# Kernel optimization log

Hardware: AMD Instinct MI355X
Metric: run time of the kernel (lower is better)

Reference implementation:

```python
import jax, jax.numpy as jnp
import numpy as np

S, T, F, J, E, H = 1024, 64, 128, 64, 256, 4
DH = E // H


def layer_norm(x, g, b, eps=1e-10):
    m = jnp.mean(x, axis=-1, keepdims=True)
    v = jnp.mean((x - m) ** 2, axis=-1, keepdims=True)  # population var (correction=0)
    return (x - m) / jnp.sqrt(v + eps) * g + b


def mha(x, Wq, Wk, Wv):
    # x: [B, L, E]; Wq/Wk/Wv: [H, E, DH]. Non-standard: scale AFTER softmax@V.
    q = jnp.einsum('ble,hed->hbld', x, Wq)
    k = jnp.einsum('ble,hed->hbld', x, Wk)
    v = jnp.einsum('ble,hed->hbld', x, Wv)
    w = jax.nn.softmax(jnp.einsum('hbld,hbmd->hblm', q, k), axis=-1)
    o = jnp.einsum('hblm,hbmd->hbld', w, v) / jnp.sqrt(jnp.asarray(Wq.shape[-1], x.dtype))
    h, b, l, d = o.shape
    return jnp.transpose(o, (1, 2, 0, 3)).reshape(b, l, h * d)


def ffn(x, W1, b1, W2, b2):
    return jnp.maximum(x @ W1 + b1, 0.0) @ W2 + b2  # Dropout is identity in eval


def pos_encoding(t, e):
    pos = jnp.arange(t, dtype=jnp.float32)[:, None]
    two_i = jnp.floor(jnp.arange(e, dtype=jnp.float32) / 2.0) * 2.0
    div = jnp.power(jnp.float32(100004.0), two_i / e)
    pe = pos / div  # [t, e]
    pe = pe.at[:, 0::2].set(jnp.sin(pe[:, 0::2]))
    pe = pe.at[:, 1::2].set(jnp.cos(pe[:, 1::2]))
    return pe


def setup_inputs() -> dict:
    key = jax.random.key(0)
    ks = jax.random.split(key, 32)
    s = 0.02
    d = {}
    d['x'] = jax.random.normal(ks[0], (S, T, F + J), dtype=jnp.float32)
    d['gate_W'] = s * jax.random.normal(ks[1], (J, F))
    d['gate_b'] = s * jax.random.normal(ks[2], (F,))
    d['embed_W'] = s * jax.random.normal(ks[3], (F, E))
    d['ln0_g'] = 1.0 + s * jax.random.normal(ks[4], (E,))
    d['ln0_b'] = s * jax.random.normal(ks[5], (E,))
    d['intra_Wq'] = s * jax.random.normal(ks[6], (H, E, DH))
    d['intra_Wk'] = s * jax.random.normal(ks[7], (H, E, DH))
    d['intra_Wv'] = s * jax.random.normal(ks[8], (H, E, DH))
    d['intra_ln_g'] = 1.0 + s * jax.random.normal(ks[9], (E,))
    d['intra_ln_b'] = s * jax.random.normal(ks[10], (E,))
    d['intra_W1'] = s * jax.random.normal(ks[11], (E, 4 * E))
    d['intra_b1'] = s * jax.random.normal(ks[12], (4 * E,))
    d['intra_W2'] = s * jax.random.normal(ks[13], (4 * E, E))
    d['intra_b2'] = s * jax.random.normal(ks[14], (E,))
    d['inter_Wq'] = s * jax.random.normal(ks[15], (H, E, DH))
    d['inter_Wk'] = s * jax.random.normal(ks[16], (H, E, DH))
    d['inter_Wv'] = s * jax.random.normal(ks[17], (H, E, DH))
    d['inter_ln1_g'] = 1.0 + s * jax.random.normal(ks[18], (E,))
    d['inter_ln1_b'] = s * jax.random.normal(ks[19], (E,))
    d['inter_ln2_g'] = 1.0 + s * jax.random.normal(ks[20], (E,))
    d['inter_ln2_b'] = s * jax.random.normal(ks[21], (E,))
    d['inter_W1'] = s * jax.random.normal(ks[22], (E, 4 * E))
    d['inter_b1'] = s * jax.random.normal(ks[23], (4 * E,))
    d['inter_W2'] = s * jax.random.normal(ks[24], (4 * E, E))
    d['inter_b2'] = s * jax.random.normal(ks[25], (E,))
    d['temp_W'] = s * jax.random.normal(ks[26], (E, E))
    d['pred_W'] = s * jax.random.normal(ks[27], (E, 1))
    d['pred_b'] = s * jax.random.normal(ks[28], (1,))
    return d


def reference(x, gate_W, gate_b, embed_W, ln0_g, ln0_b,
              intra_Wq, intra_Wk, intra_Wv, intra_ln_g, intra_ln_b,
              intra_W1, intra_b1, intra_W2, intra_b2,
              inter_Wq, inter_Wk, inter_Wv, inter_ln1_g, inter_ln1_b,
              inter_ln2_g, inter_ln2_b, inter_W1, inter_b1, inter_W2, inter_b2,
              temp_W, pred_W, pred_b):
    # Gating
    x_f = x[..., :F]                       # [S, T, F]
    x_g = x[..., -1, F:]                   # [S, J]
    gate = jax.nn.softmax(x_g @ gate_W + gate_b, axis=-1)[:, None, :]
    x_f = gate * x_f
    # Embed + positional encoding + LN
    emb = x_f @ embed_W                    # [S, T, E]
    res = emb + pos_encoding(T, E)
    ln = layer_norm(res, ln0_g, ln0_b)
    # Intra-stock attention (attend over time axis per stock)
    a = mha(ln, intra_Wq, intra_Wk, intra_Wv)
    r = a + ln
    intra_out = r + ffn(layer_norm(r, intra_ln_g, intra_ln_b), intra_W1, intra_b1, intra_W2, intra_b2)
    # Inter-stock attention (attend over stock axis per timestep)
    xT = jnp.transpose(intra_out, (1, 0, 2))            # [T, S, E]
    xTn = layer_norm(xT, inter_ln1_g, inter_ln1_b)
    a2 = mha(xTn, inter_Wq, inter_Wk, inter_Wv)          # [T, S, E]
    out = jnp.transpose(a2, (1, 0, 2))                   # [S, T, E]
    r2 = out + intra_out
    inter_out = r2 + ffn(layer_norm(r2, inter_ln2_g, inter_ln2_b), inter_W1, inter_b1, inter_W2, inter_b2)
    # Temporal aggregation
    x1 = inter_out @ temp_W                              # [S, T, E]
    cur = x1[..., -1, :][..., :, None]                   # [S, E, 1]
    lam = jax.nn.softmax(jnp.squeeze(x1 @ cur, -1), axis=-1)[:, None, :]  # [S, 1, T]
    agg = jnp.squeeze(lam @ inter_out, -2)               # [S, E]
    # Prediction
    return agg @ pred_W + pred_b                         # [S, 1]
```

## Files before the change

kernel.cpp:

```cpp
#include <hip/hip_runtime.h>


typedef _Float16 h16;
typedef __attribute__((ext_vector_type(8))) _Float16 f16x8;
typedef __attribute__((ext_vector_type(4))) _Float16 f16x4;
typedef __attribute__((ext_vector_type(4))) float f32x4;

__device__ inline float wave_sum(float v){
  #pragma unroll
  for (int o=32;o;o>>=1) v += __shfl_xor(v,o);
  return v;
}
__device__ inline float wave_max(float v){
  #pragma unroll
  for (int o=32;o;o>>=1) v = fmaxf(v,__shfl_xor(v,o));
  return v;
}

__global__ __launch_bounds__(256) void k_pe(float* __restrict__ pe){
  int t = blockIdx.x, i = threadIdx.x;
  float two_i = (float)((i>>1)<<1);
  float dv = powf(100004.0f, two_i*(1.0f/256.0f));
  float v = (float)t / dv;
  pe[t*256+i] = (i&1) ? cosf(v) : sinf(v);
}

__global__ __launch_bounds__(64) void k_gate(const float* __restrict__ x,
    const float* __restrict__ gW, const float* __restrict__ gb,
    float* __restrict__ gate){
  int s = blockIdx.x, lane = threadIdx.x;
  __shared__ float xg[64];
  xg[lane] = x[((size_t)s*64+63)*192 + 128 + lane];
  __syncthreads();
  float a0 = gb[lane], a1 = gb[64+lane];
  #pragma unroll 4
  for (int j=0;j<64;j++){
    float xv = xg[j];
    a0 += xv*gW[j*128+lane];
    a1 += xv*gW[j*128+64+lane];
  }
  float mx = wave_max(fmaxf(a0,a1));
  float e0 = __expf(a0-mx), e1 = __expf(a1-mx);
  float sm = wave_sum(e0+e1);
  gate[s*128+lane]    = e0/sm;
  gate[s*128+64+lane] = e1/sm;
}

__global__ __launch_bounds__(256) void k_t16all(
    const float* __restrict__ q1, const float* __restrict__ k1, const float* __restrict__ v1,
    const float* __restrict__ q2, const float* __restrict__ k2, const float* __restrict__ v2,
    const float* __restrict__ embed_W, const float* __restrict__ temp_W,
    const float* __restrict__ iW1, const float* __restrict__ iW2,
    const float* __restrict__ eW1, const float* __restrict__ eW2,
    h16* __restrict__ base){
  __shared__ float tile[32][33];
  const int b = blockIdx.x, tid = threadIdx.x;
  const float* src; h16* dst; int K, N, tb; bool qkv = false;
  if (b < 384){
    int mat = b>>6; tb = b&63; qkv = true; K = 256; N = 256;
    src = (mat==0)?q1:(mat==1)?k1:(mat==2)?v1:(mat==3)?q2:(mat==4)?k2:v2;
    dst = base + mat*65536;
  } else if (b < 416){ tb = b-384;  K=128;  N=256;  src=embed_W; dst=base+393216; }
  else if (b < 480){ tb = b-416;  K=256;  N=256;  src=temp_W;  dst=base+425984; }
  else if (b < 736){ tb = b-480;  K=256;  N=1024; src=iW1;     dst=base+491520; }
  else if (b < 992){ tb = b-736;  K=1024; N=256;  src=iW2;     dst=base+753664; }
  else if (b < 1248){ tb = b-992; K=256;  N=1024; src=eW1;     dst=base+1015808; }
  else               { tb = b-1248; K=1024; N=256; src=eW2;    dst=base+1277952; }
  const int nt = N>>5;
  const int N0 = (tb & (nt-1))<<5;
  const int K0 = (tb/nt)<<5;
  {
    int r = tid>>3, c0 = (tid&7)<<2;
    int k = K0+r, n = N0+c0;
    const float* p = qkv ? (src + ((n>>6)<<14) + (k<<6) + (n&63))
                         : (src + (size_t)k*N + n);
    float4 v = *(const float4*)p;
    tile[r][c0]=v.x; tile[r][c0+1]=v.y; tile[r][c0+2]=v.z; tile[r][c0+3]=v.w;
  }
  __syncthreads();
  {
    int r = tid>>3, c0 = (tid&7)<<2;
    f16x4 o;
    o[0]=(h16)tile[c0][r]; o[1]=(h16)tile[c0+1][r];
    o[2]=(h16)tile[c0+2][r]; o[3]=(h16)tile[c0+3][r];
    *(f16x4*)(dst + (size_t)(N0+r)*K + K0 + c0) = o;
  }
}

__global__ __launch_bounds__(256) void k_embed(
    const float* __restrict__ x, const h16* __restrict__ Et,
    const float* __restrict__ pe, const float* __restrict__ gate,
    const float* __restrict__ g0, const float* __restrict__ b0,
    float* __restrict__ A){
  __shared__ char pool[65536];
  h16*  As  = (h16*)pool;
  float* res = (float*)pool;
  const int tid = threadIdx.x, lane = tid&63, w = tid>>6;
  const int lr = lane&15, g = lane>>4;
  const int m0 = blockIdx.x<<6;
  #pragma unroll
  for (int it=0; it<8; it++){
    int f4 = it*256 + tid;
    int row = f4>>5, c4 = (f4&31)<<2;
    float4 v = *(const float4*)(x + (size_t)(m0+row)*192 + c4);
    float4 gg = *(const float4*)(gate + (((m0+row)>>6)<<7) + c4);
    v.x*=gg.x; v.y*=gg.y; v.z*=gg.z; v.w*=gg.w;
    int idx = ((row<<7) + c4) ^ ((row&7)<<3);
    f16x4 o; o[0]=(h16)v.x; o[1]=(h16)v.y; o[2]=(h16)v.z; o[3]=(h16)v.w;
    *(f16x4*)&As[idx] = o;
  }
  __syncthreads();
  f32x4 acc[4][4];
  #pragma unroll
  for (int a=0;a<4;a++)
    #pragma unroll
    for (int b=0;b<4;b++) acc[a][b] = (f32x4){0,0,0,0};
  #pragma unroll
  for (int kt=0; kt<4; kt++){
    f16x8 af[4], bf[4];
    #pragma unroll
    for (int rf=0; rf<4; rf++){
      int r = (rf<<4) + lr;
      int idx = ((r<<7) + (kt<<5) + (g<<3)) ^ ((r&7)<<3);
      af[rf] = *(const f16x8*)&As[idx];
    }
    #pragma unroll
    for (int cf=0; cf<4; cf++){
      int n = (w<<6) + (cf<<4) + lr;
      bf[cf] = *(const f16x8*)(Et + (size_t)n*128 + (kt<<5) + (g<<3));
    }
    #pragma unroll
    for (int rf=0; rf<4; rf++)
      #pragma unroll
      for (int cf=0; cf<4; cf++)
        acc[rf][cf] = __builtin_amdgcn_mfma_f32_16x16x32_f16(af[rf], bf[cf], acc[rf][cf], 0,0,0);
  }
  __syncthreads();
  #pragma unroll
  for (int cf=0; cf<4; cf++){
    int col = (w<<6) + (cf<<4) + lr;
    #pragma unroll
    for (int rf=0; rf<4; rf++)
      #pragma unroll
      for (int i=0;i<4;i++){
        int r = (rf<<4) + (g<<2) + i;
        res[(r<<8) + col] = acc[rf][cf][i] + pe[(r<<8) + col];
      }
  }
  __syncthreads();
  {
    float4 gg = *(const float4*)(g0 + (lane<<2));
    float4 bb = *(const float4*)(b0 + (lane<<2));
    for (int rr=0; rr<16; rr++){
      int r = (w<<4) + rr;
      float4 v = *(float4*)&res[(r<<8) + (lane<<2)];
      float sm = wave_sum(v.x+v.y+v.z+v.w);
      float sq = wave_sum(v.x*v.x+v.y*v.y+v.z*v.z+v.w*v.w);
      float mean = sm*(1.f/256.f);
      float rs = rsqrtf(sq*(1.f/256.f) - mean*mean + 1e-10f);
      float4 o;
      o.x=(v.x-mean)*rs*gg.x+bb.x; o.y=(v.y-mean)*rs*gg.y+bb.y;
      o.z=(v.z-mean)*rs*gg.z+bb.z; o.w=(v.w-mean)*rs*gg.w+bb.w;
      *(float4*)(A + (size_t)(m0+r)*256 + (lane<<2)) = o;
    }
  }
}

template<bool DOLN>
__global__ __launch_bounds__(512) void k_qkv(
    const float* __restrict__ X,
    const float* __restrict__ lng, const float* __restrict__ lnb,
    const h16* __restrict__ Bt0,
    h16* __restrict__ Qh, h16* __restrict__ Kh, h16* __restrict__ Vh){
  __shared__ h16 Xs[64*256];
  const int tid = threadIdx.x, lane = tid&63, w = tid>>6;
  const int lr = lane&15, g = lane>>4;
  const int m0 = blockIdx.x<<6;
  {
    float4 gg, bb;
    if (DOLN){ gg = *(const float4*)(lng + (lane<<2)); bb = *(const float4*)(lnb + (lane<<2)); }
    #pragma unroll
    for (int rr=0; rr<8; rr++){
      int r = (w<<3) + rr;
      float4 v = *(const float4*)(X + (size_t)(m0+r)*256 + (lane<<2));
      if (DOLN){
        float sm = wave_sum(v.x+v.y+v.z+v.w);
        float sq = wave_sum(v.x*v.x+v.y*v.y+v.z*v.z+v.w*v.w);
        float mean = sm*(1.f/256.f);
        float rs = rsqrtf(sq*(1.f/256.f) - mean*mean + 1e-10f);
        v.x=(v.x-mean)*rs*gg.x+bb.x; v.y=(v.y-mean)*rs*gg.y+bb.y;
        v.z=(v.z-mean)*rs*gg.z+bb.z; v.w=(v.w-mean)*rs*gg.w+bb.w;
      }
      f16x4 o; o[0]=(h16)v.x; o[1]=(h16)v.y; o[2]=(h16)v.z; o[3]=(h16)v.w;
      int idx = ((r<<8) + (lane<<2)) ^ ((r&7)<<3);
      *(f16x4*)&Xs[idx] = o;
    }
  }
  __syncthreads();
  f32x4 acc[4][3];
  #pragma unroll
  for (int a=0;a<4;a++)
    #pragma unroll
    for (int m=0;m<3;m++) acc[a][m] = (f32x4){0,0,0,0};
  #pragma unroll
  for (int kt=0; kt<8; kt++){
    f16x8 af[4], bf[3];
    #pragma unroll
    for (int rf=0; rf<4; rf++){
      int r = (rf<<4) + lr;
      int idx = ((r<<8) + (kt<<5) + (g<<3)) ^ ((r&7)<<3);
      af[rf] = *(const f16x8*)&Xs[idx];
    }
    #pragma unroll
    for (int m=0;m<3;m++){
      int n = (w<<4) + lr;
      bf[m] = *(const f16x8*)(Bt0 + (size_t)m*65536 + (size_t)n*256 + (kt<<5) + (g<<3));
    }
    #pragma unroll
    for (int rf=0; rf<4; rf++)
      #pragma unroll
      for (int m=0;m<3;m++)
        acc[rf][m] = __builtin_amdgcn_mfma_f32_16x16x32_f16(af[rf], bf[m], acc[rf][m], 0,0,0);
  }
  const int col = (w<<4) + lr;
  #pragma unroll
  for (int m=0;m<3;m++){
    h16* dst = (m==0)?Qh:(m==1)?Kh:Vh;
    #pragma unroll
    for (int rf=0; rf<4; rf++)
      #pragma unroll
      for (int i=0;i<4;i++){
        int r = m0 + (rf<<4) + (g<<2) + i;
        dst[(size_t)r*128 + col] = (h16)acc[rf][m][i];
      }
  }
}

template<int KDIM, int NB, int MODE>
__global__ __launch_bounds__(256) void k_gemm16(
    const float* __restrict__ A, int lda,
    const h16* __restrict__ Bt,
    void* __restrict__ Cv,
    const float* __restrict__ pe, const float* __restrict__ gate,
    size_t bstride, size_t cstride){
  __shared__ h16 As[64*KDIM];
  const int tid = threadIdx.x, lane = tid&63, w = tid>>6;
  const int lr = lane&15, g = lane>>4;
  const int m0 = blockIdx.x<<6;
  Bt += (size_t)blockIdx.y * bstride;
  constexpr int CF = NB/64;
  constexpr int KT = KDIM/32;
  #pragma unroll
  for (int it=0; it<16; it++){
    int f4 = it*256 + tid;
    int row = f4>>6, c4 = (f4&63)<<2;
    float4 v = *(const float4*)(A + (size_t)(m0+row)*lda + c4);
    int idx = ((row<<8) + c4) ^ ((row&7)<<3);
    f16x4 o; o[0]=(h16)v.x; o[1]=(h16)v.y; o[2]=(h16)v.z; o[3]=(h16)v.w;
    *(f16x4*)&As[idx] = o;
  }
  __syncthreads();
  f32x4 acc[4][CF];
  #pragma unroll
  for (int rf=0;rf<4;rf++)
    #pragma unroll
    for (int cf=0;cf<CF;cf++) acc[rf][cf] = (f32x4){0,0,0,0};
  #pragma unroll
  for (int kt=0; kt<KT; kt++){
    f16x8 af[4], bf[CF];
    #pragma unroll
    for (int rf=0; rf<4; rf++){
      int r = (rf<<4) + lr;
      int idx = (r*KDIM + (kt<<5) + (g<<3)) ^ ((r&7)<<3);
      af[rf] = *(const f16x8*)&As[idx];
    }
    #pragma unroll
    for (int cf=0; cf<CF; cf++){
      int n = w*(NB/4) + (cf<<4) + lr;
      bf[cf] = *(const f16x8*)(Bt + (size_t)n*KDIM + (kt<<5) + (g<<3));
    }
    #pragma unroll
    for (int rf=0; rf<4; rf++)
      #pragma unroll
      for (int cf=0; cf<CF; cf++)
        acc[rf][cf] = __builtin_amdgcn_mfma_f32_16x16x32_f16(af[rf], bf[cf], acc[rf][cf], 0,0,0);
  }
  #pragma unroll
  for (int cf=0; cf<CF; cf++){
    int col = w*(NB/4) + (cf<<4) + lr;
    #pragma unroll
    for (int rf=0; rf<4; rf++)
      #pragma unroll
      for (int i=0;i<4;i++){
        int m = m0 + (rf<<4) + (g<<2) + i;
        ((float*)Cv)[(size_t)m*256 + col] = acc[rf][cf][i];
      }
  }
}

template<int NT, int QG>
__global__ __launch_bounds__(256) void k_attn16(
    const h16* __restrict__ Qh, const h16* __restrict__ Kh, const h16* __restrict__ Vh,
    const float* __restrict__ Resid, float* __restrict__ Out, int hbase){
  __shared__ h16 Ks[64*64];
  __shared__ h16 VsT[64*64];
  __shared__ h16 Ps[4*QG*16*64];
  const int tid = threadIdx.x, lane = tid&63, w = tid>>6;
  const int lr = lane&15, g = lane>>4;
  int hh, t=0, qc=0, s=0;
  if (NT==1){ s = blockIdx.x; hh = blockIdx.y; }
  else      { hh = blockIdx.x; t = blockIdx.y; qc = blockIdx.z; }
  const int ccol = hh<<6;
  const int gcol = (hbase+hh)<<6;

  f16x8 qf[QG][2];
  #pragma unroll
  for (int grp=0; grp<QG; grp++){
    int ql = grp*64 + (w<<4) + lr;
    size_t m = (NT==1) ? ((size_t)s*64 + ql) : (((size_t)qc*(64*QG) + ql)*64 + t);
    const h16* qp = Qh + m*128 + ccol + (g<<3);
    qf[grp][0] = *(const f16x8*)qp;
    qf[grp][1] = *(const f16x8*)(qp + 32);
  }

  f32x4 oc[QG][4];
  float m_r[QG], l_r[QG];
  #pragma unroll
  for (int grp=0; grp<QG; grp++){
    #pragma unroll
    for (int cf=0;cf<4;cf++) oc[grp][cf] = (f32x4){0,0,0,0};
    m_r[grp] = -1e30f; l_r[grp] = 0.f;
  }

  for (int kb=0; kb<NT; kb++){
    __syncthreads();
    #pragma unroll
    for (int it=0; it<2; it++){
      int u = it*256 + tid;
      int row = u>>3, un = u&7;
      size_t m = (NT==1) ? ((size_t)s*64 + row) : (((size_t)kb*64 + row)*64 + t);
      f16x8 kv = *(const f16x8*)(Kh + m*128 + ccol + (un<<3));
      *(f16x8*)&Ks[(row<<6) + ((un ^ (row&7))<<3)] = kv;
      f16x8 vv = *(const f16x8*)(Vh + m*128 + ccol + (un<<3));
      #pragma unroll
      for (int j=0;j<8;j++){
        int d = (un<<3) + j;
        int key = (d + un) & 7;
        VsT[(d<<6) + ((((row>>3) ^ key))<<3) + (row&7)] = vv[j];
      }
    }
    __syncthreads();
    #pragma unroll
    for (int grp=0; grp<QG; grp++){
      f32x4 sa[4];
      #pragma unroll
      for (int mm=0;mm<4;mm++) sa[mm] = (f32x4){0,0,0,0};
      #pragma unroll
      for (int ks=0; ks<2; ks++){
        #pragma unroll
        for (int mm=0;mm<4;mm++){
          int krow = (mm<<4) + lr;
          f16x8 af = *(const f16x8*)&Ks[(krow<<6) + (((g + (ks<<2)) ^ (krow&7))<<3)];
          sa[mm] = __builtin_amdgcn_mfma_f32_16x16x32_f16(af, qf[grp][ks], sa[mm], 0,0,0);
        }
      }
      float pmax = -1e30f;
      #pragma unroll
      for (int mm=0;mm<4;mm++)
        #pragma unroll
        for (int i=0;i<4;i++) pmax = fmaxf(pmax, sa[mm][i]);
      pmax = fmaxf(pmax, __shfl_xor(pmax, 16));
      pmax = fmaxf(pmax, __shfl_xor(pmax, 32));
      float mn = fmaxf(m_r[grp], pmax);
      float sca = __expf(m_r[grp] - mn);
      m_r[grp] = mn;
      float ps = 0.f;
      f16x4 pv[4];
      #pragma unroll
      for (int mm=0;mm<4;mm++){
        #pragma unroll
        for (int i=0;i<4;i++){
          float p = __expf(sa[mm][i] - mn);
          ps += p;
          pv[mm][i] = (h16)p;
        }
      }
      ps += __shfl_xor(ps, 16);
      ps += __shfl_xor(ps, 32);
      l_r[grp] = l_r[grp]*sca + ps;
      const int pbase = ((w*QG + grp)<<10);
      #pragma unroll
      for (int mm=0;mm<4;mm++){
        int k0 = (mm<<4) + (g<<2);
        int unit = k0>>3, off = k0&7;
        *(f16x4*)&Ps[pbase + (lr<<6) + ((unit ^ (lr&7))<<3) + off] = pv[mm];
      }
      #pragma unroll
      for (int i=0;i<4;i++){
        float si = __shfl(sca, (g<<4) + (g<<2) + i);
        #pragma unroll
        for (int cf=0;cf<4;cf++) oc[grp][cf][i] *= si;
      }
      #pragma unroll
      for (int ks=0; ks<2; ks++){
        f16x8 pa = *(const f16x8*)&Ps[pbase + (lr<<6) + (((g + (ks<<2)) ^ (lr&7))<<3)];
        #pragma unroll
        for (int cf=0;cf<4;cf++){
          int d = (cf<<4) + lr;
          int key = (d + (d>>3)) & 7;
          f16x8 bf = *(const f16x8*)&VsT[(d<<6) + (((g + (ks<<2)) ^ key)<<3)];
          oc[grp][cf] = __builtin_amdgcn_mfma_f32_16x16x32_f16(pa, bf, oc[grp][cf], 0,0,0);
        }
      }
    }
  }
  #pragma unroll
  for (int grp=0; grp<QG; grp++){
    float linv = 1.0f/(l_r[grp]*8.0f);
    #pragma unroll
    for (int i=0;i<4;i++){
      float li = __shfl(linv, (g<<4) + (g<<2) + i);
      int ql = grp*64 + (w<<4) + (g<<2) + i;
      size_t m = (NT==1) ? ((size_t)s*64 + ql) : (((size_t)qc*(64*QG) + ql)*64 + t);
      #pragma unroll
      for (int cf=0;cf<4;cf++){
        int d = (cf<<4) + lr;
        size_t ga = m*256 + gcol + d;
        Out[ga] = oc[grp][cf][i]*li + Resid[ga];
      }
    }
  }
}

__global__ __launch_bounds__(512) void k_ffn2(
    const float* X, float* Out,
    const float* __restrict__ lng, const float* __restrict__ lnb,
    const h16* __restrict__ W1t, const float* __restrict__ b1,
    const h16* __restrict__ W2t, const float* __restrict__ b2){
  __shared__ h16 Xs[64*256];
  __shared__ h16 Hc[64*256];
  const int tid  = threadIdx.x;
  const int lane = tid & 63;
  const int w    = tid >> 6;
  const int r0   = blockIdx.x << 6;
  const int lr   = lane & 15;
  const int g    = lane >> 4;
  {
    float4 gg = *(const float4*)(lng + (lane<<2));
    float4 bb = *(const float4*)(lnb + (lane<<2));
    #pragma unroll
    for (int rr=0; rr<8; rr++){
      int r = (w<<3) + rr;
      float4 v = *(const float4*)(X + (size_t)(r0+r)*256 + (lane<<2));
      float sm = wave_sum(v.x+v.y+v.z+v.w);
      float sq = wave_sum(v.x*v.x+v.y*v.y+v.z*v.z+v.w*v.w);
      float mean = sm*(1.f/256.f);
      float rs = rsqrtf(sq*(1.f/256.f) - mean*mean + 1e-10f);
      f16x4 o;
      o[0]=(h16)((v.x-mean)*rs*gg.x+bb.x); o[1]=(h16)((v.y-mean)*rs*gg.y+bb.y);
      o[2]=(h16)((v.z-mean)*rs*gg.z+bb.z); o[3]=(h16)((v.w-mean)*rs*gg.w+bb.w);
      int idx = ((r<<8) + (lane<<2)) ^ ((r&7)<<3);
      *(f16x4*)&Xs[idx] = o;
    }
  }
  __syncthreads();
  f32x4 acc2[4][2];
  #pragma unroll
  for (int a=0;a<4;a++){ acc2[a][0]=(f32x4){0,0,0,0}; acc2[a][1]=(f32x4){0,0,0,0}; }
  for (int hc=0; hc<4; hc++){
    f32x4 acc1[4][2];
    #pragma unroll
    for (int a=0;a<4;a++){ acc1[a][0]=(f32x4){0,0,0,0}; acc1[a][1]=(f32x4){0,0,0,0}; }
    #pragma unroll
    for (int kt=0; kt<8; kt++){
      f16x8 af[4], bf[2];
      #pragma unroll
      for (int rf=0; rf<4; rf++){
        int r = (rf<<4) + lr;
        int idx = ((r<<8) + (kt<<5) + (g<<3)) ^ ((r&7)<<3);
        af[rf] = *(const f16x8*)&Xs[idx];
      }
      #pragma unroll
      for (int cf=0; cf<2; cf++){
        int n = (hc<<8) + (w<<5) + (cf<<4) + lr;
        bf[cf] = *(const f16x8*)(W1t + (size_t)n*256 + (kt<<5) + (g<<3));
      }
      #pragma unroll
      for (int rf=0; rf<4; rf++)
        #pragma unroll
        for (int cf=0; cf<2; cf++)
          acc1[rf][cf] = __builtin_amdgcn_mfma_f32_16x16x32_f16(
              af[rf], bf[cf], acc1[rf][cf], 0, 0, 0);
    }
    __syncthreads();
    #pragma unroll
    for (int cf=0; cf<2; cf++){
      int cl = (w<<5) + (cf<<4) + lr;
      float bv = b1[(hc<<8) + cl];
      #pragma unroll
      for (int rf=0; rf<4; rf++){
        #pragma unroll
        for (int i=0;i<4;i++){
          int r = (rf<<4) + (g<<2) + i;
          float hv = fmaxf(acc1[rf][cf][i] + bv, 0.f);
          int idx = ((r<<8) + cl) ^ ((r&7)<<3);
          Hc[idx] = (h16)hv;
        }
      }
    }
    __syncthreads();
    #pragma unroll
    for (int kt=0; kt<8; kt++){
      f16x8 af[4], bf[2];
      #pragma unroll
      for (int rf=0; rf<4; rf++){
        int r = (rf<<4) + lr;
        int idx = ((r<<8) + (kt<<5) + (g<<3)) ^ ((r&7)<<3);
        af[rf] = *(const f16x8*)&Hc[idx];
      }
      #pragma unroll
      for (int cf=0; cf<2; cf++){
        int n = (w<<5) + (cf<<4) + lr;
        bf[cf] = *(const f16x8*)(W2t + (size_t)n*1024 + (hc<<8) + (kt<<5) + (g<<3));
      }
      #pragma unroll
      for (int rf=0; rf<4; rf++)
        #pragma unroll
        for (int cf=0; cf<2; cf++)
          acc2[rf][cf] = __builtin_amdgcn_mfma_f32_16x16x32_f16(
              af[rf], bf[cf], acc2[rf][cf], 0, 0, 0);
    }
  }
  #pragma unroll
  for (int cf=0; cf<2; cf++){
    int col = (w<<5) + (cf<<4) + lr;
    float bv = b2[col];
    #pragma unroll
    for (int rf=0; rf<4; rf++){
      #pragma unroll
      for (int i=0;i<4;i++){
        size_t r = (size_t)r0 + (rf<<4) + (g<<2) + i;
        float res = X[r*256 + col];
        Out[r*256 + col] = acc2[rf][cf][i] + bv + res;
      }
    }
  }
}

__global__ __launch_bounds__(256) void k_final2(const float* __restrict__ IO,
    const float* __restrict__ X1, const float* __restrict__ predW,
    const float* __restrict__ predb, float* __restrict__ out){
  const int s = blockIdx.x, tid = threadIdx.x;
  __shared__ float cur[256];
  __shared__ float lam[64];
  __shared__ float red[4];
  const int wv = tid>>6, lane = tid&63;
  cur[tid] = X1[((size_t)(s*64+63))*256 + tid];
  __syncthreads();
  float lg[16];
  for (int r=0;r<16;r++){
    int trow = wv*16+r;
    float4 xa = *(const float4*)(X1 + ((size_t)(s*64+trow))*256 + (lane<<2));
    float4 xc = *(float4*)&cur[lane<<2];
    lg[r] = wave_sum(xa.x*xc.x + xa.y*xc.y + xa.z*xc.z + xa.w*xc.w);
  }
  if (lane==0){
    #pragma unroll
    for (int r=0;r<16;r++) lam[wv*16+r] = lg[r];
  }
  __syncthreads();
  if (tid < 64){
    float v = lam[tid];
    float mx = wave_max(v);
    float p = __expf(v-mx);
    float sm = wave_sum(p);
    lam[tid] = p/sm;
  }
  __syncthreads();
  float ag = 0.f;
  for (int tt=0;tt<64;tt++)
    ag += lam[tt]*IO[((size_t)(s*64+tt))*256 + tid];
  float wsum = wave_sum(ag * predW[tid]);
  if (lane==0) red[wv] = wsum;
  __syncthreads();
  if (tid==0) out[s] = red[0]+red[1]+red[2]+red[3] + predb[0];
}

extern "C" void kernel_launch(void* const* d_in, const int* in_sizes, int n_in,
                              void* d_out, int out_size, void* d_ws, size_t ws_size,
                              hipStream_t stream){
  const float* x       = (const float*)d_in[0];
  const float* gate_W  = (const float*)d_in[1];
  const float* gate_b  = (const float*)d_in[2];
  const float* embed_W = (const float*)d_in[3];
  const float* ln0_g   = (const float*)d_in[4];
  const float* ln0_b   = (const float*)d_in[5];
  const float* iln_g   = (const float*)d_in[9];
  const float* iln_b   = (const float*)d_in[10];
  const float* iW1     = (const float*)d_in[11];
  const float* ib1     = (const float*)d_in[12];
  const float* iW2     = (const float*)d_in[13];
  const float* ib2     = (const float*)d_in[14];
  const float* eln1_g  = (const float*)d_in[18];
  const float* eln1_b  = (const float*)d_in[19];
  const float* eln2_g  = (const float*)d_in[20];
  const float* eln2_b  = (const float*)d_in[21];
  const float* eW1     = (const float*)d_in[22];
  const float* eb1     = (const float*)d_in[23];
  const float* eW2     = (const float*)d_in[24];
  const float* eb2     = (const float*)d_in[25];
  const float* temp_W  = (const float*)d_in[26];
  const float* pred_W  = (const float*)d_in[27];
  const float* pred_b  = (const float*)d_in[28];
  float* out = (float*)d_out;

  float* pe    = (float*)d_ws;
  float* gate  = pe + 16384;
  h16* fQKV = (h16*)((char*)d_ws + ((size_t)4<<20));
  h16* fE   = fQKV + 393216;
  h16* fT   = fE + 32768;
  h16* fW1i = fT + 65536;
  h16* fW2i = fW1i + 262144;
  h16* fW1e = fW2i + 262144;
  h16* fW2e = fW1e + 262144;
  const size_t MR = (size_t)65536*256, MH = (size_t)65536*128;
  float* A  = (float*)((char*)d_ws + ((size_t)8<<20));
  float* Bb = A + MR;
  h16* Qh = (h16*)(Bb + MR);
  h16* Kh = Qh + MH;
  h16* Vh = Kh + MH;

  k_pe  <<<64,  256, 0, stream>>>(pe);
  k_gate<<<1024, 64, 0, stream>>>(x, gate_W, gate_b, gate);
  k_t16all<<<1504,256,0,stream>>>(
      (const float*)d_in[6],(const float*)d_in[7],(const float*)d_in[8],
      (const float*)d_in[15],(const float*)d_in[16],(const float*)d_in[17],
      embed_W, temp_W, iW1, iW2, eW1, eW2, fQKV);

  k_embed<<<1024,256,0,stream>>>(x, fE, pe, gate, ln0_g, ln0_b, A);

  for (int hp=0; hp<2; hp++){
    int hb = hp*2;
    k_qkv<false><<<1024,512,0,stream>>>(A, nullptr, nullptr,
        fQKV + hb*16384, Qh, Kh, Vh);
    k_attn16<1,1><<<dim3(1024,2),256,0,stream>>>(Qh, Kh, Vh, A, Bb, hb);
  }
  k_ffn2<<<1024,512,0,stream>>>(Bb, Bb, iln_g, iln_b, fW1i, ib1, fW2i, ib2);

  for (int hp=0; hp<2; hp++){
    int hb = hp*2;
    k_qkv<true><<<1024,512,0,stream>>>(Bb, eln1_g, eln1_b,
        fQKV + 3*65536 + hb*16384, Qh, Kh, Vh);
    k_attn16<16,2><<<dim3(2,64,8),256,0,stream>>>(Qh, Kh, Vh, Bb, Bb, hb);
  }
  k_ffn2<<<1024,512,0,stream>>>(Bb, Bb, eln2_g, eln2_b, fW1e, eb1, fW2e, eb2);

  k_gemm16<256,256,2><<<1024,256,0,stream>>>(Bb, 256, fT, A, nullptr, nullptr, 0, 0);
  k_final2<<<1024,256,0,stream>>>(Bb, A, pred_W, pred_b, out);
}
```

Baseline: 870.5 us.

## Retile FFN to 32-row blocks with double-buffered hidden tile and W2 prefetch

After: 987.7 us. 13.5% more time.

```diff
diff --git a/kernel.cpp b/kernel.cpp
--- a/kernel.cpp
+++ b/kernel.cpp
@@ -432,19 +432,20 @@
   }
 }
 
-__global__ __launch_bounds__(512) void k_ffn2(
+__global__ __launch_bounds__(256) void k_ffn3(
     const float* X, float* Out,
     const float* __restrict__ lng, const float* __restrict__ lnb,
     const h16* __restrict__ W1t, const float* __restrict__ b1,
     const h16* __restrict__ W2t, const float* __restrict__ b2){
-  __shared__ h16 Xs[64*256];
-  __shared__ h16 Hc[64*256];
+  __shared__ h16 Xs[32*256];
+  __shared__ h16 Hc[2][32*256];
   const int tid  = threadIdx.x;
   const int lane = tid & 63;
   const int w    = tid >> 6;
-  const int r0   = blockIdx.x << 6;
+  const int r0   = blockIdx.x << 5;
   const int lr   = lane & 15;
   const int g    = lane >> 4;
+
   {
     float4 gg = *(const float4*)(lng + (lane<<2));
     float4 bb = *(const float4*)(lnb + (lane<<2));
@@ -464,79 +465,96 @@
     }
   }
   __syncthreads();
-  f32x4 acc2[4][2];
-  #pragma unroll
-  for (int a=0;a<4;a++){ acc2[a][0]=(f32x4){0,0,0,0}; acc2[a][1]=(f32x4){0,0,0,0}; }
+
+  f32x4 acc2[2][4];
+  #pragma unroll
+  for (int a=0;a<2;a++)
+    #pragma unroll
+    for (int b=0;b<4;b++) acc2[a][b] = (f32x4){0,0,0,0};
+
   for (int hc=0; hc<4; hc++){
-    f32x4 acc1[4][2];
-    #pragma unroll
-    for (int a=0;a<4;a++){ acc1[a][0]=(f32x4){0,0,0,0}; acc1[a][1]=(f32x4){0,0,0,0}; }
+    f32x4 acc1[2][4];
+    #pragma unroll
+    for (int a=0;a<2;a++)
+      #pragma unroll
+      for (int b=0;b<4;b++) acc1[a][b] = (f32x4){0,0,0,0};
     #pragma unroll
     for (int kt=0; kt<8; kt++){
-      f16x8 af[4], bf[2];
-      #pragma unroll
-      for (int rf=0; rf<4; rf++){
+      f16x8 af[2], bf[4];
+      #pragma unroll
+      for (int rf=0; rf<2; rf++){
         int r = (rf<<4) + lr;
         int idx = ((r<<8) + (kt<<5) + (g<<3)) ^ ((r&7)<<3);
         af[rf] = *(const f16x8*)&Xs[idx];
       }
       #pragma unroll
-      for (int cf=0; cf<2; cf++){
-        int n = (hc<<8) + (w<<5) + (cf<<4) + lr;
+      for (int cf=0; cf<4; cf++){
+        int n = (hc<<8) + (w<<6) + (cf<<4) + lr;
         bf[cf] = *(const f16x8*)(W1t + (size_t)n*256 + (kt<<5) + (g<<3));
       }
       #pragma unroll
-      for (int rf=0; rf<4; rf++)
-        #pragma unroll
-        for (int cf=0; cf<2; cf++)
+      for (int rf=0; rf<2; rf++)
+        #pragma unroll
+        for (int cf=0; cf<4; cf++)
           acc1[rf][cf] = __builtin_amdgcn_mfma_f32_16x16x32_f16(
               af[rf], bf[cf], acc1[rf][cf], 0, 0, 0);
     }
-    __syncthreads();
-    #pragma unroll
-    for (int cf=0; cf<2; cf++){
-      int cl = (w<<5) + (cf<<4) + lr;
+    f16x8 pf[4];
+    #pragma unroll
+    for (int cf=0; cf<4; cf++){
+      int n = (w<<6) + (cf<<4) + lr;
+      pf[cf] = *(const f16x8*)(W2t + (size_t)n*1024 + (hc<<8) + (g<<3));
+    }
+    h16* Hb = Hc[hc&1];
+    #pragma unroll
+    for (int cf=0; cf<4; cf++){
+      int cl = (w<<6) + (cf<<4) + lr;
       float bv = b1[(hc<<8) + cl];
       #pragma unroll
-      for (int rf=0; rf<4; rf++){
+      for (int rf=0; rf<2; rf++){
         #pragma unroll
         for (int i=0;i<4;i++){
           int r = (rf<<4) + (g<<2) + i;
           float hv = fmaxf(acc1[rf][cf][i] + bv, 0.f);
           int idx = ((r<<8) + cl) ^ ((r&7)<<3);
-          Hc[idx] = (h16)hv;
+          Hb[idx] = (h16)hv;
         }
       }
     }
     __syncthreads();
     #pragma unroll
     for (int kt=0; kt<8; kt++){
-      f16x8 af[4], bf[2];
-      #pragma unroll
-      for (int rf=0; rf<4; rf++){
+      f16x8 af[2], bf[4];
+      #pragma unroll
+      for (int rf=0; rf<2; rf++){
         int r = (rf<<4) + lr;
         int idx = ((r<<8) + (kt<<5) + (g<<3)) ^ ((r&7)<<3);
-        af[rf] = *(const f16x8*)&Hc[idx];
-      }
-      #pragma unroll
-      for (int cf=0; cf<2; cf++){
-        int n = (w<<5) + (cf<<4) + lr;
-        bf[cf] = *(const f16x8*)(W2t + (size_t)n*1024 + (hc<<8) + (kt<<5) + (g<<3));
-      }
-      #pragma unroll
-      for (int rf=0; rf<4; rf++)
-        #pragma unroll
-        for (int cf=0; cf<2; cf++)
+        af[rf] = *(const f16x8*)&Hb[idx];
+      }
+      if (kt==0){
+        #pragma unroll
+        for (int cf=0; cf<4; cf++) bf[cf] = pf[cf];
+      } else {
+        #pragma unroll
+        for (int cf=0; cf<4; cf++){
+          int n = (w<<6) + (cf<<4) + lr;
+          bf[cf] = *(const f16x8*)(W2t + (size_t)n*1024 + (hc<<8) + (kt<<5) + (g<<3));
+        }
+      }
+      #pragma unroll
+      for (int rf=0; rf<2; rf++)
+        #pragma unroll
+        for (int cf=0; cf<4; cf++)
           acc2[rf][cf] = __builtin_amdgcn_mfma_f32_16x16x32_f16(
               af[rf], bf[cf], acc2[rf][cf], 0, 0, 0);
     }
   }
   #pragma unroll
-  for (int cf=0; cf<2; cf++){
-    int col = (w<<5) + (cf<<4) + lr;
+  for (int cf=0; cf<4; cf++){
+    int col = (w<<6) + (cf<<4) + lr;
     float bv = b2[col];
     #pragma unroll
-    for (int rf=0; rf<4; rf++){
+    for (int rf=0; rf<2; rf++){
       #pragma unroll
       for (int i=0;i<4;i++){
         size_t r = (size_t)r0 + (rf<<4) + (g<<2) + i;
@@ -645,15 +663,15 @@
         fQKV + hb*16384, Qh, Kh, Vh);
     k_attn16<1,1><<<dim3(1024,2),256,0,stream>>>(Qh, Kh, Vh, A, Bb, hb);
   }
-  k_ffn2<<<1024,512,0,stream>>>(Bb, Bb, iln_g, iln_b, fW1i, ib1, fW2i, ib2);
+  k_ffn3<<<2048,256,0,stream>>>(Bb, Bb, iln_g, iln_b, fW1i, ib1, fW2i, ib2);
 
   for (int hp=0; hp<2; hp++){
     int hb = hp*2;
     k_qkv<true><<<1024,512,0,stream>>>(Bb, eln1_g, eln1_b,
         fQKV + 3*65536 + hb*16384, Qh, Kh, Vh);
-    k_attn16<16,2><<<dim3(2,64,8),256,0,stream>>>(Qh, Kh, Vh, Bb, Bb, hb);
-  }
-  k_ffn2<<<1024,512,0,stream>>>(Bb, Bb, eln2_g, eln2_b, fW1e, eb1, fW2e, eb2);
+    k_attn16<16,1><<<dim3(2,64,16),256,0,stream>>>(Qh, Kh, Vh, Bb, Bb, hb);
+  }
+  k_ffn3<<<2048,256,0,stream>>>(Bb, Bb, eln2_g, eln2_b, fW1e, eb1, fW2e, eb2);
 
   k_gemm16<256,256,2><<<1024,256,0,stream>>>(Bb, 256, fT, A, nullptr, nullptr, 0, 0);
   k_final2<<<1024,256,0,stream>>>(Bb, A, pred_W, pred_b, out);
```

## Materialize full FFN hidden tile in LDS and split inter-attention grid finer

Applied to the files above, without the earlier changes.

New measurement: 793.4 us. 8.8% less time.

```diff
diff --git a/kernel.cpp b/kernel.cpp
--- a/kernel.cpp
+++ b/kernel.cpp
@@ -236,18 +236,15 @@
   }
 }
 
-template<int KDIM, int NB, int MODE>
+template<int KDIM, int NB>
 __global__ __launch_bounds__(256) void k_gemm16(
     const float* __restrict__ A, int lda,
     const h16* __restrict__ Bt,
-    void* __restrict__ Cv,
-    const float* __restrict__ pe, const float* __restrict__ gate,
-    size_t bstride, size_t cstride){
+    float* __restrict__ Cv){
   __shared__ h16 As[64*KDIM];
   const int tid = threadIdx.x, lane = tid&63, w = tid>>6;
   const int lr = lane&15, g = lane>>4;
   const int m0 = blockIdx.x<<6;
-  Bt += (size_t)blockIdx.y * bstride;
   constexpr int CF = NB/64;
   constexpr int KT = KDIM/32;
   #pragma unroll
@@ -293,7 +290,7 @@
       #pragma unroll
       for (int i=0;i<4;i++){
         int m = m0 + (rf<<4) + (g<<2) + i;
-        ((float*)Cv)[(size_t)m*256 + col] = acc[rf][cf][i];
+        Cv[(size_t)m*256 + col] = acc[rf][cf][i];
       }
   }
 }
@@ -432,19 +429,20 @@
   }
 }
 
-__global__ __launch_bounds__(512) void k_ffn2(
+__global__ __launch_bounds__(512,1) void k_ffn4(
     const float* X, float* Out,
     const float* __restrict__ lng, const float* __restrict__ lnb,
     const h16* __restrict__ W1t, const float* __restrict__ b1,
     const h16* __restrict__ W2t, const float* __restrict__ b2){
   __shared__ h16 Xs[64*256];
-  __shared__ h16 Hc[64*256];
+  __shared__ h16 Hc[64*1024];
   const int tid  = threadIdx.x;
   const int lane = tid & 63;
   const int w    = tid >> 6;
   const int r0   = blockIdx.x << 6;
   const int lr   = lane & 15;
   const int g    = lane >> 4;
+
   {
     float4 gg = *(const float4*)(lng + (lane<<2));
     float4 bb = *(const float4*)(lnb + (lane<<2));
@@ -464,16 +462,16 @@
     }
   }
   __syncthreads();
-  f32x4 acc2[4][2];
-  #pragma unroll
-  for (int a=0;a<4;a++){ acc2[a][0]=(f32x4){0,0,0,0}; acc2[a][1]=(f32x4){0,0,0,0}; }
-  for (int hc=0; hc<4; hc++){
-    f32x4 acc1[4][2];
-    #pragma unroll
-    for (int a=0;a<4;a++){ acc1[a][0]=(f32x4){0,0,0,0}; acc1[a][1]=(f32x4){0,0,0,0}; }
+
+  {
+    f32x4 acc1[4][8];
+    #pragma unroll
+    for (int a=0;a<4;a++)
+      #pragma unroll
+      for (int b=0;b<8;b++) acc1[a][b] = (f32x4){0,0,0,0};
     #pragma unroll
     for (int kt=0; kt<8; kt++){
-      f16x8 af[4], bf[2];
+      f16x8 af[4], bf[8];
       #pragma unroll
       for (int rf=0; rf<4; rf++){
         int r = (rf<<4) + lr;
@@ -481,55 +479,58 @@
         af[rf] = *(const f16x8*)&Xs[idx];
       }
       #pragma unroll
-      for (int cf=0; cf<2; cf++){
-        int n = (hc<<8) + (w<<5) + (cf<<4) + lr;
+      for (int cf=0; cf<8; cf++){
+        int n = (w<<7) + (cf<<4) + lr;
         bf[cf] = *(const f16x8*)(W1t + (size_t)n*256 + (kt<<5) + (g<<3));
       }
       #pragma unroll
       for (int rf=0; rf<4; rf++)
         #pragma unroll
-        for (int cf=0; cf<2; cf++)
+        for (int cf=0; cf<8; cf++)
           acc1[rf][cf] = __builtin_amdgcn_mfma_f32_16x16x32_f16(
               af[rf], bf[cf], acc1[rf][cf], 0, 0, 0);
     }
-    __syncthreads();
-    #pragma unroll
-    for (int cf=0; cf<2; cf++){
-      int cl = (w<<5) + (cf<<4) + lr;
-      float bv = b1[(hc<<8) + cl];
+    #pragma unroll
+    for (int cf=0; cf<8; cf++){
+      int cl = (w<<7) + (cf<<4) + lr;
+      float bv = b1[cl];
       #pragma unroll
       for (int rf=0; rf<4; rf++){
         #pragma unroll
         for (int i=0;i<4;i++){
           int r = (rf<<4) + (g<<2) + i;
           float hv = fmaxf(acc1[rf][cf][i] + bv, 0.f);
-          int idx = ((r<<8) + cl) ^ ((r&7)<<3);
+          int idx = ((r<<10) + cl) ^ ((r&7)<<3);
           Hc[idx] = (h16)hv;
         }
       }
     }
-    __syncthreads();
-    #pragma unroll
-    for (int kt=0; kt<8; kt++){
-      f16x8 af[4], bf[2];
-      #pragma unroll
-      for (int rf=0; rf<4; rf++){
-        int r = (rf<<4) + lr;
-        int idx = ((r<<8) + (kt<<5) + (g<<3)) ^ ((r&7)<<3);
-        af[rf] = *(const f16x8*)&Hc[idx];
-      }
-      #pragma unroll
-      for (int cf=0; cf<2; cf++){
-        int n = (w<<5) + (cf<<4) + lr;
-        bf[cf] = *(const f16x8*)(W2t + (size_t)n*1024 + (hc<<8) + (kt<<5) + (g<<3));
-      }
-      #pragma unroll
-      for (int rf=0; rf<4; rf++)
-        #pragma unroll
-        for (int cf=0; cf<2; cf++)
-          acc2[rf][cf] = __builtin_amdgcn_mfma_f32_16x16x32_f16(
-              af[rf], bf[cf], acc2[rf][cf], 0, 0, 0);
-    }
+  }
+  __syncthreads();
+
+  f32x4 acc2[4][2];
+  #pragma unroll
+  for (int a=0;a<4;a++){ acc2[a][0]=(f32x4){0,0,0,0}; acc2[a][1]=(f32x4){0,0,0,0}; }
+  #pragma unroll 4
+  for (int kt=0; kt<32; kt++){
+    f16x8 af[4], bf[2];
+    #pragma unroll
+    for (int rf=0; rf<4; rf++){
+      int r = (rf<<4) + lr;
+      int idx = ((r<<10) + (kt<<5) + (g<<3)) ^ ((r&7)<<3);
+      af[rf] = *(const f16x8*)&Hc[idx];
+    }
+    #pragma unroll
+    for (int cf=0; cf<2; cf++){
+      int n = (w<<5) + (cf<<4) + lr;
+      bf[cf] = *(const f16x8*)(W2t + (size_t)n*1024 + (kt<<5) + (g<<3));
+    }
+    #pragma unroll
+    for (int rf=0; rf<4; rf++)
+      #pragma unroll
+      for (int cf=0; cf<2; cf++)
+        acc2[rf][cf] = __builtin_amdgcn_mfma_f32_16x16x32_f16(
+            af[rf], bf[cf], acc2[rf][cf], 0, 0, 0);
   }
   #pragma unroll
   for (int cf=0; cf<2; cf++){
@@ -645,16 +646,16 @@
         fQKV + hb*16384, Qh, Kh, Vh);
     k_attn16<1,1><<<dim3(1024,2),256,0,stream>>>(Qh, Kh, Vh, A, Bb, hb);
   }
-  k_ffn2<<<1024,512,0,stream>>>(Bb, Bb, iln_g, iln_b, fW1i, ib1, fW2i, ib2);
+  k_ffn4<<<1024,512,0,stream>>>(Bb, Bb, iln_g, iln_b, fW1i, ib1, fW2i, ib2);
 
   for (int hp=0; hp<2; hp++){
     int hb = hp*2;
     k_qkv<true><<<1024,512,0,stream>>>(Bb, eln1_g, eln1_b,
         fQKV + 3*65536 + hb*16384, Qh, Kh, Vh);
-    k_attn16<16,2><<<dim3(2,64,8),256,0,stream>>>(Qh, Kh, Vh, Bb, Bb, hb);
-  }
-  k_ffn2<<<1024,512,0,stream>>>(Bb, Bb, eln2_g, eln2_b, fW1e, eb1, fW2e, eb2);
-
-  k_gemm16<256,256,2><<<1024,256,0,stream>>>(Bb, 256, fT, A, nullptr, nullptr, 0, 0);
+    k_attn16<16,1><<<dim3(2,64,16),256,0,stream>>>(Qh, Kh, Vh, Bb, Bb, hb);
+  }
+  k_ffn4<<<1024,512,0,stream>>>(Bb, Bb, eln2_g, eln2_b, fW1e, eb1, fW2e, eb2);
+
+  k_gemm16<256,256><<<1024,256,0,stream>>>(Bb, 256, fT, A);
   k_final2<<<1024,256,0,stream>>>(Bb, A, pred_W, pred_b, out);
 }
```
